# Kernel optimization log

Hardware: AMD Instinct MI355X
Metric: run time of the kernel (lower is better)

The kernel has to match this reference:

```python
import jax, jax.numpy as jnp
import numpy as np

R = 16
ALPHA = 32
SCALING = ALPHA / R
SLOTS = 32
IN_F = 4096
OUT_F = 4096
B, T = 8, 1024


def setup_inputs() -> dict:
    key = jax.random.key(0)
    k1, k2, k3, k4, k5, k6 = jax.random.split(key, 6)
    x = jax.random.normal(k1, (B, T, IN_F), dtype=jnp.float32)
    adapter_mapping = jax.random.randint(k2, (B,), 0, SLOTS, dtype=jnp.int32)
    W = jax.random.normal(k3, (OUT_F, IN_F), dtype=jnp.float32) * 0.02
    b = jax.random.normal(k4, (OUT_F,), dtype=jnp.float32) * 0.02
    lora_As = jax.random.normal(k5, (SLOTS, IN_F, R), dtype=jnp.float32) * 0.02
    lora_Bs = jax.random.normal(k6, (SLOTS, R, OUT_F), dtype=jnp.float32) * 0.02
    return {"x": x, "adapter_mapping": adapter_mapping, "W": W, "b": b,
            "lora_As": lora_As, "lora_Bs": lora_Bs}


def reference(x, adapter_mapping, W, b, lora_As, lora_Bs):
    # base linear: y = x @ W.T + b
    base_out = jnp.einsum('bti,oi->bto', x, W) + b
    # per-example adapter gather (index_select along slot dim)
    A = lora_As[adapter_mapping]          # [B, in, r]
    Bm = lora_Bs[adapter_mapping]         # [B, r, out]
    lora_h = jnp.einsum('bti,bir->btr', x, A)
    lora_out = jnp.einsum('btr,bro->bto', lora_h, Bm)
    return base_out + lora_out * SCALING
```

## Files before the change

### kernel.cpp

```cpp
#include <hip/hip_runtime.h>
#include <hip/hip_bf16.h>


typedef __bf16 bf16_t;
typedef __bf16 bf16x8 __attribute__((ext_vector_type(8)));
typedef __bf16 bf16x4 __attribute__((ext_vector_type(4)));
typedef float f32x4 __attribute__((ext_vector_type(4)));

#define M_DIM 8192
#define K_DIM 4096
#define N_DIM 4096
#define SCALE_F 2.0f

__device__ __forceinline__ void gload_lds16(const void* g, void* l) {
    __builtin_amdgcn_global_load_lds(
        (const __attribute__((address_space(1))) void*)g,
        (__attribute__((address_space(3))) void*)l, 16, 0, 0);
}

__global__ __launch_bounds__(256) void cvt_kernel(const float* __restrict__ src,
                                                  bf16_t* __restrict__ dst, int n4) {
    int i = blockIdx.x * 256 + threadIdx.x;
    const int stride = gridDim.x * 256;
    for (; i < n4; i += stride) {
        f32x4 v = ((const f32x4*)src)[i];
        bf16x4 o = {(bf16_t)v[0], (bf16_t)v[1], (bf16_t)v[2], (bf16_t)v[3]};
        ((bf16x4*)dst)[i] = o;
    }
}

__global__ __launch_bounds__(256) void lora_h_kernel(
    const float* __restrict__ X,
    const float* __restrict__ lora_As,
    const int* __restrict__ mapping,
    float* __restrict__ h_ws,
    bf16_t* __restrict__ Xb)
{
    __shared__ float AT[256 * 16];
    __shared__ float XT[16 * 256];
    const int tid  = threadIdx.x;
    const int wave = tid >> 6;
    const int lane = tid & 63;
    const int m0   = blockIdx.x * 16;
    const int slot = mapping[m0 >> 10];
    const float* __restrict__ A = lora_As + (size_t)slot * K_DIM * 16;

    float h[4][4];
#pragma unroll
    for (int i = 0; i < 4; ++i)
#pragma unroll
        for (int c = 0; c < 4; ++c) h[i][c] = 0.f;

    for (int k0 = 0; k0 < K_DIM; k0 += 256) {
#pragma unroll
        for (int c = 0; c < 4; ++c) {
            const int u = tid + 256 * c;
            f32x4 v = *(const f32x4*)(A + (size_t)k0 * 16 + u * 4);
            *(f32x4*)(AT + u * 4) = v;
        }
#pragma unroll
        for (int c = 0; c < 4; ++c) {
            const int u = tid + 256 * c;
            const int row = u >> 6, ch = u & 63;
            const size_t goff = (size_t)(m0 + row) * K_DIM + k0 + ch * 4;
            f32x4 v = *(const f32x4*)(X + goff);
            *(f32x4*)(XT + row * 256 + ch * 4) = v;
            if (Xb) {
                bf16x4 o = {(bf16_t)v[0], (bf16_t)v[1], (bf16_t)v[2], (bf16_t)v[3]};
                *(bf16x4*)(Xb + goff) = o;
            }
        }
        __syncthreads();
#pragma unroll 4
        for (int s = 0; s < 16; ++s) {
            f32x4 av = *(const f32x4*)(AT + s * 256 + lane * 4);
#pragma unroll
            for (int i = 0; i < 4; ++i) {
                const float xv = XT[(wave * 4 + i) * 256 + s * 16 + (lane >> 2)];
#pragma unroll
                for (int c = 0; c < 4; ++c) h[i][c] += xv * av[c];
            }
        }
        __syncthreads();
    }
#pragma unroll
    for (int i = 0; i < 4; ++i)
#pragma unroll
        for (int c = 0; c < 4; ++c) {
            float v = h[i][c];
            v += __shfl_xor(v, 4, 64);
            v += __shfl_xor(v, 8, 64);
            v += __shfl_xor(v, 16, 64);
            v += __shfl_xor(v, 32, 64);
            h[i][c] = v * SCALE_F;
        }
    if (lane < 4) {
#pragma unroll
        for (int i = 0; i < 4; ++i) {
            f32x4 o = {h[i][0], h[i][1], h[i][2], h[i][3]};
            *(f32x4*)(h_ws + (size_t)(m0 + wave * 4 + i) * 16 + lane * 4) = o;
        }
    }
}

__device__ __forceinline__ void epilogue(
    f32x4 (&acc)[4][4], const float* __restrict__ bias,
    const float* __restrict__ lora_Bs, const int* __restrict__ mapping,
    const float* __restrict__ h_ws, float* __restrict__ out,
    int bm0, int bn0, int wm0, int wn0, int r16, int kq)
{
    const int slot = mapping[bm0 >> 10];
    const bool hasK = (kq < 2);
    const int kq2 = hasK ? kq : 0;

    bf16x8 hfrag[4], bmf[4];
#pragma unroll
    for (int i = 0; i < 4; ++i) {
        const float* hp = h_ws + (size_t)(bm0 + wm0 + i * 16 + r16) * 16 + kq2 * 8;
        f32x4 h0 = *(const f32x4*)hp;
        f32x4 h1 = *(const f32x4*)(hp + 4);
#pragma unroll
        for (int jj = 0; jj < 4; ++jj) {
            hfrag[i][jj]     = hasK ? (bf16_t)h0[jj] : (bf16_t)0.f;
            hfrag[i][jj + 4] = hasK ? (bf16_t)h1[jj] : (bf16_t)0.f;
        }
    }
#pragma unroll
    for (int j = 0; j < 4; ++j) {
        const int o = bn0 + wn0 + j * 16 + r16;
#pragma unroll
        for (int jj = 0; jj < 8; ++jj) {
            const int r = kq2 * 8 + jj;
            const float v = lora_Bs[((size_t)slot * 16 + r) * N_DIM + o];
            bmf[j][jj] = hasK ? (bf16_t)v : (bf16_t)0.f;
        }
    }
#pragma unroll
    for (int i = 0; i < 4; ++i)
#pragma unroll
        for (int j = 0; j < 4; ++j)
            acc[i][j] = __builtin_amdgcn_mfma_f32_16x16x32_bf16(hfrag[i], bmf[j], acc[i][j], 0, 0, 0);

#pragma unroll
    for (int j = 0; j < 4; ++j) {
        const int o = bn0 + wn0 + j * 16 + r16;
        const float bv = bias[o];
#pragma unroll
        for (int i = 0; i < 4; ++i) {
#pragma unroll
            for (int e = 0; e < 4; ++e) {
                const int m = bm0 + wm0 + i * 16 + kq * 4 + e;
                out[(size_t)m * N_DIM + o] = acc[i][j][e] + bv;
            }
        }
    }
}

__global__ __launch_bounds__(256) void gemm_lora_direct(
    const bf16_t* __restrict__ Xb, const bf16_t* __restrict__ Wb,
    const float* __restrict__ bias, const float* __restrict__ lora_Bs,
    const int* __restrict__ mapping, const float* __restrict__ h_ws,
    float* __restrict__ out)
{
    __shared__ bf16_t As[128 * 64];
    __shared__ bf16_t Bs[128 * 64];

    const int tid  = threadIdx.x;
    const int wave = tid >> 6;
    const int lane = tid & 63;
    const int bid  = blockIdx.x;
    const int n_t  = (bid & 7) + ((bid >> 9) << 3);
    const int m_t  = (bid >> 3) & 63;
    const int bm0 = m_t * 128;
    const int bn0 = n_t * 128;
    const int wm0 = (wave >> 1) * 64;
    const int wn0 = (wave & 1) * 64;
    const int r16 = lane & 15;
    const int kq  = lane >> 4;

    f32x4 acc[4][4];
#pragma unroll
    for (int i = 0; i < 4; ++i)
#pragma unroll
        for (int j = 0; j < 4; ++j) acc[i][j] = (f32x4){0.f, 0.f, 0.f, 0.f};

    for (int k0 = 0; k0 < K_DIM; k0 += 64) {
#pragma unroll
        for (int p = 0; p < 4; ++p) {
            const int base = wave * 256 + p * 64;
            const int s    = base + lane;
            const int row  = s >> 3;
            const int k8g  = (s & 7) ^ (row & 7);
            gload_lds16(Xb + (size_t)(bm0 + row) * K_DIM + k0 + k8g * 8,
                        As + (size_t)base * 8);
            gload_lds16(Wb + (size_t)(bn0 + row) * K_DIM + k0 + k8g * 8,
                        Bs + (size_t)base * 8);
        }
        __syncthreads();

#pragma unroll
        for (int kh = 0; kh < 2; ++kh) {
            bf16x8 af[4], bfr[4];
            const int k8 = kh * 4 + kq;
#pragma unroll
            for (int i = 0; i < 4; ++i) {
                const int ra = wm0 + i * 16 + r16;
                const int rb = wn0 + i * 16 + r16;
                af[i]  = *(const bf16x8*)(As + ((size_t)ra * 8 + (k8 ^ (ra & 7))) * 8);
                bfr[i] = *(const bf16x8*)(Bs + ((size_t)rb * 8 + (k8 ^ (rb & 7))) * 8);
            }
#pragma unroll
            for (int i = 0; i < 4; ++i)
#pragma unroll
                for (int j = 0; j < 4; ++j)
                    acc[i][j] = __builtin_amdgcn_mfma_f32_16x16x32_bf16(af[i], bfr[j], acc[i][j], 0, 0, 0);
        }
        __syncthreads();
    }

    epilogue(acc, bias, lora_Bs, mapping, h_ws, out, bm0, bn0, wm0, wn0, r16, kq);
}

__global__ __launch_bounds__(256) void gemm_lora_f32s(
    const float* __restrict__ Xf, const float* __restrict__ Wf,
    const float* __restrict__ bias, const float* __restrict__ lora_Bs,
    const int* __restrict__ mapping, const float* __restrict__ h_ws,
    float* __restrict__ out)
{
    __shared__ float Asf[128 * 32];
    __shared__ float Bsf[128 * 32];

    const int tid  = threadIdx.x;
    const int wave = tid >> 6;
    const int lane = tid & 63;
    const int bid  = blockIdx.x;
    const int n_t  = (bid & 7) + ((bid >> 9) << 3);
    const int m_t  = (bid >> 3) & 63;
    const int bm0 = m_t * 128;
    const int bn0 = n_t * 128;
    const int wm0 = (wave >> 1) * 64;
    const int wn0 = (wave & 1) * 64;
    const int r16 = lane & 15;
    const int kq  = lane >> 4;

    f32x4 acc[4][4];
#pragma unroll
    for (int i = 0; i < 4; ++i)
#pragma unroll
        for (int j = 0; j < 4; ++j) acc[i][j] = (f32x4){0.f, 0.f, 0.f, 0.f};

    for (int k0 = 0; k0 < K_DIM; k0 += 32) {
#pragma unroll
        for (int p = 0; p < 4; ++p) {
            const int idx0 = (p * 4 + wave) * 64;
            const int idx  = idx0 + lane;
            const int k4   = idx >> 7;
            const int row  = idx & 127;
            gload_lds16(Xf + (size_t)(bm0 + row) * K_DIM + (k0 + k4 * 4),
                        Asf + (size_t)idx0 * 4);
            gload_lds16(Wf + (size_t)(bn0 + row) * K_DIM + (k0 + k4 * 4),
                        Bsf + (size_t)idx0 * 4);
        }
        __syncthreads();

        bf16x8 af[4], bfr[4];
#pragma unroll
        for (int i = 0; i < 4; ++i) {
            const int ra = wm0 + i * 16 + r16;
            const int rb = wn0 + i * 16 + r16;
            f32x4 a0 = *(const f32x4*)(Asf + ((size_t)(kq * 2) * 128 + ra) * 4);
            f32x4 a1 = *(const f32x4*)(Asf + ((size_t)(kq * 2 + 1) * 128 + ra) * 4);
            f32x4 b0 = *(const f32x4*)(Bsf + ((size_t)(kq * 2) * 128 + rb) * 4);
            f32x4 b1 = *(const f32x4*)(Bsf + ((size_t)(kq * 2 + 1) * 128 + rb) * 4);
            af[i]  = (bf16x8){(bf16_t)a0[0], (bf16_t)a0[1], (bf16_t)a0[2], (bf16_t)a0[3],
                              (bf16_t)a1[0], (bf16_t)a1[1], (bf16_t)a1[2], (bf16_t)a1[3]};
            bfr[i] = (bf16x8){(bf16_t)b0[0], (bf16_t)b0[1], (bf16_t)b0[2], (bf16_t)b0[3],
                              (bf16_t)b1[0], (bf16_t)b1[1], (bf16_t)b1[2], (bf16_t)b1[3]};
        }
#pragma unroll
        for (int i = 0; i < 4; ++i)
#pragma unroll
            for (int j = 0; j < 4; ++j)
                acc[i][j] = __builtin_amdgcn_mfma_f32_16x16x32_bf16(af[i], bfr[j], acc[i][j], 0, 0, 0);
        __syncthreads();
    }

    epilogue(acc, bias, lora_Bs, mapping, h_ws, out, bm0, bn0, wm0, wn0, r16, kq);
}

extern "C" void kernel_launch(void* const* d_in, const int* in_sizes, int n_in,
                              void* d_out, int out_size, void* d_ws, size_t ws_size,
                              hipStream_t stream) {
    const float* x        = (const float*)d_in[0];
    const int*   mapping  = (const int*)d_in[1];
    const float* W        = (const float*)d_in[2];
    const float* b        = (const float*)d_in[3];
    const float* lora_As  = (const float*)d_in[4];
    const float* lora_Bs  = (const float*)d_in[5];
    float* out = (float*)d_out;

    const size_t xb_bytes = (size_t)M_DIM * K_DIM * 2;
    const size_t wb_bytes = (size_t)N_DIM * K_DIM * 2;
    const size_t h_bytes  = (size_t)M_DIM * 16 * 4;
    const bool direct = ws_size >= xb_bytes + wb_bytes + h_bytes;

    bf16_t* Xb = (bf16_t*)d_ws;
    bf16_t* Wb = (bf16_t*)((char*)d_ws + xb_bytes);
    float*  h_ws = direct ? (float*)((char*)d_ws + xb_bytes + wb_bytes)
                          : (float*)d_ws;

    lora_h_kernel<<<dim3(M_DIM / 16), 256, 0, stream>>>(
        x, lora_As, mapping, h_ws, direct ? Xb : nullptr);

    if (direct) {
        cvt_kernel<<<dim3(2048), 256, 0, stream>>>(W, Wb, N_DIM * K_DIM / 4);
        gemm_lora_direct<<<dim3(2048), 256, 0, stream>>>(
            Xb, Wb, b, lora_Bs, mapping, h_ws, out);
    } else {
        gemm_lora_f32s<<<dim3(2048), 256, 0, stream>>>(
            x, W, b, lora_Bs, mapping, h_ws, out);
    }
}
```

Before: 644.0 us.

## Compute LoRA down-projection with bf16 MFMA and 32-row tiles

```diff
diff --git a/kernel.cpp b/kernel.cpp
--- a/kernel.cpp
+++ b/kernel.cpp
@@ -29,77 +29,90 @@
     }
 }
 
-__global__ __launch_bounds__(256) void lora_h_kernel(
+__global__ __launch_bounds__(256) void lora_hx_kernel(
     const float* __restrict__ X,
     const float* __restrict__ lora_As,
     const int* __restrict__ mapping,
     float* __restrict__ h_ws,
     bf16_t* __restrict__ Xb)
 {
-    __shared__ float AT[256 * 16];
-    __shared__ float XT[16 * 256];
+    __shared__ bf16_t Xt[32 * 16 * 8];
+    __shared__ bf16_t At[16 * 136];
+    __shared__ float hred[4 * 2 * 16 * 16];
+
     const int tid  = threadIdx.x;
     const int wave = tid >> 6;
     const int lane = tid & 63;
-    const int m0   = blockIdx.x * 16;
-    const int slot = mapping[m0 >> 10];
-    const float* __restrict__ A = lora_As + (size_t)slot * K_DIM * 16;
-
-    float h[4][4];
-#pragma unroll
-    for (int i = 0; i < 4; ++i)
-#pragma unroll
-        for (int c = 0; c < 4; ++c) h[i][c] = 0.f;
-
-    for (int k0 = 0; k0 < K_DIM; k0 += 256) {
-#pragma unroll
-        for (int c = 0; c < 4; ++c) {
-            const int u = tid + 256 * c;
-            f32x4 v = *(const f32x4*)(A + (size_t)k0 * 16 + u * 4);
-            *(f32x4*)(AT + u * 4) = v;
-        }
-#pragma unroll
-        for (int c = 0; c < 4; ++c) {
-            const int u = tid + 256 * c;
-            const int row = u >> 6, ch = u & 63;
-            const size_t goff = (size_t)(m0 + row) * K_DIM + k0 + ch * 4;
-            f32x4 v = *(const f32x4*)(X + goff);
-            *(f32x4*)(XT + row * 256 + ch * 4) = v;
-            if (Xb) {
-                bf16x4 o = {(bf16_t)v[0], (bf16_t)v[1], (bf16_t)v[2], (bf16_t)v[3]};
-                *(bf16x4*)(Xb + goff) = o;
+    const int bm0  = blockIdx.x * 32;
+    const int slot = mapping[bm0 >> 10];
+    const float* __restrict__ A = lora_As + (size_t)slot * (K_DIM * 16);
+
+    const int srow = tid >> 3;
+    const int sc2  = tid & 7;
+    const int r16  = lane & 15;
+    const int kq   = lane >> 4;
+
+    f32x4 acc[2];
+    acc[0] = (f32x4){0.f, 0.f, 0.f, 0.f};
+    acc[1] = (f32x4){0.f, 0.f, 0.f, 0.f};
+
+    for (int k0 = 0; k0 < K_DIM; k0 += 128) {
+        const float* xp = X + (size_t)(bm0 + srow) * K_DIM + k0 + sc2 * 16;
+        f32x4 v0 = *(const f32x4*)(xp);
+        f32x4 v1 = *(const f32x4*)(xp + 4);
+        f32x4 v2 = *(const f32x4*)(xp + 8);
+        f32x4 v3 = *(const f32x4*)(xp + 12);
+        bf16x8 c0 = {(bf16_t)v0[0], (bf16_t)v0[1], (bf16_t)v0[2], (bf16_t)v0[3],
+                     (bf16_t)v1[0], (bf16_t)v1[1], (bf16_t)v1[2], (bf16_t)v1[3]};
+        bf16x8 c1 = {(bf16_t)v2[0], (bf16_t)v2[1], (bf16_t)v2[2], (bf16_t)v2[3],
+                     (bf16_t)v3[0], (bf16_t)v3[1], (bf16_t)v3[2], (bf16_t)v3[3]};
+        if (Xb) {
+            bf16x8* xbp = (bf16x8*)(Xb + (size_t)(bm0 + srow) * K_DIM + k0 + sc2 * 16);
+            xbp[0] = c0;
+            xbp[1] = c1;
+        }
+        const int k8a = sc2 * 2, k8b = sc2 * 2 + 1;
+        *(bf16x8*)(Xt + (srow * 16 + (k8a ^ (srow & 15))) * 8) = c0;
+        *(bf16x8*)(Xt + (srow * 16 + (k8b ^ (srow & 15))) * 8) = c1;
+
+        {
+            const int kk = tid >> 1, half = tid & 1;
+            const float* ap = A + (size_t)(k0 + kk) * 16 + half * 8;
+            f32x4 a0 = *(const f32x4*)ap;
+            f32x4 a1 = *(const f32x4*)(ap + 4);
+#pragma unroll
+            for (int rr = 0; rr < 4; ++rr) {
+                At[(half * 8 + rr) * 136 + kk]     = (bf16_t)a0[rr];
+                At[(half * 8 + 4 + rr) * 136 + kk] = (bf16_t)a1[rr];
             }
         }
         __syncthreads();
-#pragma unroll 4
-        for (int s = 0; s < 16; ++s) {
-            f32x4 av = *(const f32x4*)(AT + s * 256 + lane * 4);
-#pragma unroll
-            for (int i = 0; i < 4; ++i) {
-                const float xv = XT[(wave * 4 + i) * 256 + s * 16 + (lane >> 2)];
-#pragma unroll
-                for (int c = 0; c < 4; ++c) h[i][c] += xv * av[c];
-            }
-        }
-        __syncthreads();
-    }
-#pragma unroll
-    for (int i = 0; i < 4; ++i)
-#pragma unroll
-        for (int c = 0; c < 4; ++c) {
-            float v = h[i][c];
-            v += __shfl_xor(v, 4, 64);
-            v += __shfl_xor(v, 8, 64);
-            v += __shfl_xor(v, 16, 64);
-            v += __shfl_xor(v, 32, 64);
-            h[i][c] = v * SCALE_F;
-        }
-    if (lane < 4) {
-#pragma unroll
-        for (int i = 0; i < 4; ++i) {
-            f32x4 o = {h[i][0], h[i][1], h[i][2], h[i][3]};
-            *(f32x4*)(h_ws + (size_t)(m0 + wave * 4 + i) * 16 + lane * 4) = o;
-        }
+
+#pragma unroll
+        for (int i = 0; i < 2; ++i) {
+            const int row_l = i * 16 + r16;
+            const int c = wave * 4 + kq;
+            bf16x8 af  = *(const bf16x8*)(Xt + (row_l * 16 + (c ^ (row_l & 15))) * 8);
+            bf16x8 bfr = *(const bf16x8*)(At + r16 * 136 + wave * 32 + kq * 8);
+            acc[i] = __builtin_amdgcn_mfma_f32_16x16x32_bf16(af, bfr, acc[i], 0, 0, 0);
+        }
+        __syncthreads();
+    }
+
+#pragma unroll
+    for (int i = 0; i < 2; ++i)
+#pragma unroll
+        for (int e = 0; e < 4; ++e)
+            hred[wave * 512 + i * 256 + (kq * 4 + e) * 16 + r16] = acc[i][e];
+    __syncthreads();
+#pragma unroll
+    for (int q = 0; q < 2; ++q) {
+        const int entry = tid * 2 + q;
+        const int row_l = entry >> 4, col = entry & 15;
+        const int i = row_l >> 4, rr = row_l & 15;
+        const int off = i * 256 + rr * 16 + col;
+        float s = hred[off] + hred[512 + off] + hred[1024 + off] + hred[1536 + off];
+        h_ws[(size_t)(bm0 + row_l) * 16 + col] = s * SCALE_F;
     }
 }
 
@@ -309,7 +322,7 @@
     float*  h_ws = direct ? (float*)((char*)d_ws + xb_bytes + wb_bytes)
                           : (float*)d_ws;
 
-    lora_h_kernel<<<dim3(M_DIM / 16), 256, 0, stream>>>(
+    lora_hx_kernel<<<dim3(M_DIM / 32), 256, 0, stream>>>(
         x, lora_As, mapping, h_ws, direct ? Xb : nullptr);
 
     if (direct) {
```

Measured after the change: 640.7 us. No clear change (-0.5%).
